# Kernel tuning notes

Measured on AMD Instinct MI355X. Metric: run time of the kernel, lower is better.

## Reference

```python
import jax, jax.numpy as jnp
import numpy as np

N, C, T = 65536, 1000, 2.0

def setup_inputs() -> dict:
    key = jax.random.key(0)
    k1, k2, k3, k4 = jax.random.split(key, 4)
    return {
        "outputs1": jax.random.normal(k1, (N, C), dtype=jnp.float32),
        "outputs2": jax.random.normal(k2, (N, C), dtype=jnp.float32),
        "mimic": jax.random.normal(k3, (N, C), dtype=jnp.float32),
        "targets": jax.random.randint(k4, (N,), 0, C, dtype=jnp.int64),
        "n_test": N,
    }

def _margin(x, targets):
    # top-2 per row; margin = top1 - top2 if target logit equals the max, else 0
    top2, _ = jax.lax.top_k(x, 2)                       # [N, 2]
    tgt_logit = jnp.take_along_axis(x, targets[:, None], axis=1)[:, 0]  # [N]
    return jnp.where(tgt_logit == top2[:, 0], top2[:, 0] - top2[:, 1], 0.0)

def reference(outputs1, outputs2, mimic, targets, n_test):
    d1 = _margin(outputs1, targets)
    d2 = _margin(outputs2, targets)
    m = _margin(mimic, targets)
    preds = jnp.stack([d1, d2, m], axis=1)              # [N, 3]
    out_threshold = jax.nn.softmax(preds / T, axis=1)   # softmax over the 3 margins
    max_preds = jnp.maximum(outputs1.max(), outputs2.max())
    return (max_preds, out_threshold)
```

## Files before the change

kernel.cpp:

```cpp
#include <hip/hip_runtime.h>
#include <math.h>

#define NEG_INF (-__builtin_inff())

__device__ __forceinline__ void top2_update(float v, float& m1, float& m2) {
    float nm1 = fmaxf(m1, v);
    m2 = fmaxf(m2, fminf(m1, v));
    m1 = nm1;
}

__device__ __forceinline__ void upd4(float4 v, float& m1, float& m2) {
    top2_update(v.x, m1, m2); top2_update(v.y, m1, m2);
    top2_update(v.z, m1, m2); top2_update(v.w, m1, m2);
}

__device__ __forceinline__ void top2_merge(float o1, float o2, float& m1, float& m2) {
    float hi = fmaxf(m1, o1);
    float lo = fminf(m1, o1);
    m2 = fmaxf(lo, fmaxf(m2, o2));
    m1 = hi;
}

__device__ __forceinline__ unsigned int enc_float(float f) {
    unsigned int b = __float_as_uint(f);
    return (b & 0x80000000u) ? ~b : (b | 0x80000000u);
}

__global__ __launch_bounds__(256) void margin_softmax_kernel(
    const float* __restrict__ out1,
    const float* __restrict__ out2,
    const float* __restrict__ mim,
    const int*   __restrict__ targets,
    float*       __restrict__ d_out,
    int N)
{
    const int C = 1000;
    const int lane          = threadIdx.x & 63;
    const int wave_in_blk   = threadIdx.x >> 6;
    const int waves_per_blk = blockDim.x >> 6;
    const int gwave  = blockIdx.x * waves_per_blk + wave_in_blk;
    const int nwaves = gridDim.x * waves_per_blk;

    float lane_run = NEG_INF;

    for (int row = gwave; row < N; row += nwaves) {
        const size_t base = (size_t)row * (size_t)C;
        const float4* p1 = (const float4*)(out1 + base);
        const float4* p2 = (const float4*)(out2 + base);
        const float4* p3 = (const float4*)(mim  + base);

        float4 A0 = p1[lane], A1 = p1[lane + 64], A2 = p1[lane + 128];
        float4 B0 = p2[lane], B1 = p2[lane + 64], B2 = p2[lane + 128];
        float4 M0 = p3[lane], M1 = p3[lane + 64], M2 = p3[lane + 128];
        float4 A3 = make_float4(NEG_INF, NEG_INF, NEG_INF, NEG_INF);
        float4 B3 = A3, M3 = A3;
        if (lane < 58) {
            A3 = p1[lane + 192];
            B3 = p2[lane + 192];
            M3 = p3[lane + 192];
        }

        float a1 = NEG_INF, a2 = NEG_INF;
        float b1 = NEG_INF, b2 = NEG_INF;
        float c1 = NEG_INF, c2 = NEG_INF;

        upd4(A0, a1, a2); upd4(A1, a1, a2); upd4(A2, a1, a2); upd4(A3, a1, a2);
        upd4(B0, b1, b2); upd4(B1, b1, b2); upd4(B2, b1, b2); upd4(B3, b1, b2);
        upd4(M0, c1, c2); upd4(M1, c1, c2); upd4(M2, c1, c2); upd4(M3, c1, c2);

        #pragma unroll
        for (int off = 32; off >= 1; off >>= 1) {
            float o1, o2;
            o1 = __shfl_xor(a1, off); o2 = __shfl_xor(a2, off); top2_merge(o1, o2, a1, a2);
            o1 = __shfl_xor(b1, off); o2 = __shfl_xor(b2, off); top2_merge(o1, o2, b1, b2);
            o1 = __shfl_xor(c1, off); o2 = __shfl_xor(c2, off); top2_merge(o1, o2, c1, c2);
        }

        lane_run = fmaxf(lane_run, fmaxf(a1, b1));

        if (lane == 0) {
            int tgt = targets[row];
            float t1 = out1[base + tgt];
            float t2 = out2[base + tgt];
            float t3 = mim [base + tgt];
            float d1 = (t1 == a1) ? (a1 - a2) : 0.0f;
            float d2 = (t2 == b1) ? (b1 - b2) : 0.0f;
            float d3 = (t3 == c1) ? (c1 - c2) : 0.0f;
            float x1 = d1 * 0.5f, x2 = d2 * 0.5f, x3 = d3 * 0.5f;
            float mx = fmaxf(x1, fmaxf(x2, x3));
            float e1 = expf(x1 - mx), e2 = expf(x2 - mx), e3 = expf(x3 - mx);
            float inv = 1.0f / (e1 + e2 + e3);
            float* o = d_out + 1 + (size_t)row * 3;
            o[0] = e1 * inv;
            o[1] = e2 * inv;
            o[2] = e3 * inv;
        }
    }

    #pragma unroll
    for (int off = 32; off >= 1; off >>= 1)
        lane_run = fmaxf(lane_run, __shfl_xor(lane_run, off));

    __shared__ float smax[8];
    if (lane == 0) smax[wave_in_blk] = lane_run;
    __syncthreads();
    if (threadIdx.x == 0) {
        float m = smax[0];
        for (int i = 1; i < waves_per_blk; i++) m = fmaxf(m, smax[i]);
        atomicMax((unsigned int*)d_out, enc_float(m));
    }
}

__global__ void finalize_max_kernel(float* d_out) {
    unsigned int u = ((unsigned int*)d_out)[0];
    unsigned int b = (u & 0x80000000u) ? (u ^ 0x80000000u) : ~u;
    d_out[0] = __uint_as_float(b);
}

extern "C" void kernel_launch(void* const* d_in, const int* in_sizes, int n_in,
                              void* d_out, int out_size, void* d_ws, size_t ws_size,
                              hipStream_t stream) {
    const float* out1    = (const float*)d_in[0];
    const float* out2    = (const float*)d_in[1];
    const float* mim     = (const float*)d_in[2];
    const int*   targets = (const int*)  d_in[3];

    const int N = in_sizes[3];

    (void)hipMemsetAsync(d_out, 0, sizeof(unsigned int), stream);

    margin_softmax_kernel<<<2048, 256, 0, stream>>>(
        out1, out2, mim, targets, (float*)d_out, N);

    finalize_max_kernel<<<1, 1, 0, stream>>>((float*)d_out);
}
```

Measured before the change: 649.3 us.

## Software-pipeline row loads so the next row's data is fetched during current compute

```diff
diff --git a/kernel.cpp b/kernel.cpp
--- a/kernel.cpp
+++ b/kernel.cpp
@@ -14,6 +14,13 @@
     top2_update(v.z, m1, m2); top2_update(v.w, m1, m2);
 }
 
+__device__ __forceinline__ void upd4m(float4 v, bool act, float& m1, float& m2) {
+    top2_update(act ? v.x : NEG_INF, m1, m2);
+    top2_update(act ? v.y : NEG_INF, m1, m2);
+    top2_update(act ? v.z : NEG_INF, m1, m2);
+    top2_update(act ? v.w : NEG_INF, m1, m2);
+}
+
 __device__ __forceinline__ void top2_merge(float o1, float o2, float& m1, float& m2) {
     float hi = fmaxf(m1, o1);
     float lo = fminf(m1, o1);
@@ -24,6 +31,31 @@
 __device__ __forceinline__ unsigned int enc_float(float f) {
     unsigned int b = __float_as_uint(f);
     return (b & 0x80000000u) ? ~b : (b | 0x80000000u);
+}
+
+struct Pending {
+    int    tgt;
+    float4 A0, A1, A2, A3;
+    float4 B0, B1, B2, B3;
+    float4 M0, M1, M2, M3;
+};
+
+__device__ __forceinline__ Pending issue_row(const float* __restrict__ out1,
+                                             const float* __restrict__ out2,
+                                             const float* __restrict__ mim,
+                                             const int*   __restrict__ targets,
+                                             int row, int lane, int tidx)
+{
+    const size_t base = (size_t)row * 1000u;
+    const float4* p1 = (const float4*)(out1 + base);
+    const float4* p2 = (const float4*)(out2 + base);
+    const float4* p3 = (const float4*)(mim  + base);
+    Pending P;
+    P.tgt = targets[row];
+    P.A0 = p1[lane]; P.A1 = p1[lane + 64]; P.A2 = p1[lane + 128]; P.A3 = p1[tidx];
+    P.B0 = p2[lane]; P.B1 = p2[lane + 64]; P.B2 = p2[lane + 128]; P.B3 = p2[tidx];
+    P.M0 = p3[lane]; P.M1 = p3[lane + 64]; P.M2 = p3[lane + 128]; P.M3 = p3[tidx];
+    return P;
 }
 
 __global__ __launch_bounds__(256) void margin_softmax_kernel(
@@ -40,33 +72,33 @@
     const int waves_per_blk = blockDim.x >> 6;
     const int gwave  = blockIdx.x * waves_per_blk + wave_in_blk;
     const int nwaves = gridDim.x * waves_per_blk;
+    const int  tidx = (lane < 58) ? (lane + 192) : lane;
+    const bool tact = (lane < 58);
 
     float lane_run = NEG_INF;
 
-    for (int row = gwave; row < N; row += nwaves) {
+    int row = gwave;
+    Pending cur;
+    if (row < N) cur = issue_row(out1, out2, mim, targets, row, lane, tidx);
+
+    while (row < N) {
         const size_t base = (size_t)row * (size_t)C;
-        const float4* p1 = (const float4*)(out1 + base);
-        const float4* p2 = (const float4*)(out2 + base);
-        const float4* p3 = (const float4*)(mim  + base);
 
-        float4 A0 = p1[lane], A1 = p1[lane + 64], A2 = p1[lane + 128];
-        float4 B0 = p2[lane], B1 = p2[lane + 64], B2 = p2[lane + 128];
-        float4 M0 = p3[lane], M1 = p3[lane + 64], M2 = p3[lane + 128];
-        float4 A3 = make_float4(NEG_INF, NEG_INF, NEG_INF, NEG_INF);
-        float4 B3 = A3, M3 = A3;
-        if (lane < 58) {
-            A3 = p1[lane + 192];
-            B3 = p2[lane + 192];
-            M3 = p3[lane + 192];
-        }
+        const int tgt = cur.tgt;
+        float t1 = out1[base + tgt];
+        float t2 = out2[base + tgt];
+        float t3 = mim [base + tgt];
+
+        const int nrow = row + nwaves;
+        Pending nxt;
+        if (nrow < N) nxt = issue_row(out1, out2, mim, targets, nrow, lane, tidx);
 
         float a1 = NEG_INF, a2 = NEG_INF;
         float b1 = NEG_INF, b2 = NEG_INF;
         float c1 = NEG_INF, c2 = NEG_INF;
-
-        upd4(A0, a1, a2); upd4(A1, a1, a2); upd4(A2, a1, a2); upd4(A3, a1, a2);
-        upd4(B0, b1, b2); upd4(B1, b1, b2); upd4(B2, b1, b2); upd4(B3, b1, b2);
-        upd4(M0, c1, c2); upd4(M1, c1, c2); upd4(M2, c1, c2); upd4(M3, c1, c2);
+        upd4(cur.A0, a1, a2); upd4(cur.A1, a1, a2); upd4(cur.A2, a1, a2); upd4m(cur.A3, tact, a1, a2);
+        upd4(cur.B0, b1, b2); upd4(cur.B1, b1, b2); upd4(cur.B2, b1, b2); upd4m(cur.B3, tact, b1, b2);
+        upd4(cur.M0, c1, c2); upd4(cur.M1, c1, c2); upd4(cur.M2, c1, c2); upd4m(cur.M3, tact, c1, c2);
 
         #pragma unroll
         for (int off = 32; off >= 1; off >>= 1) {
@@ -79,10 +111,6 @@
         lane_run = fmaxf(lane_run, fmaxf(a1, b1));
 
         if (lane == 0) {
-            int tgt = targets[row];
-            float t1 = out1[base + tgt];
-            float t2 = out2[base + tgt];
-            float t3 = mim [base + tgt];
             float d1 = (t1 == a1) ? (a1 - a2) : 0.0f;
             float d2 = (t2 == b1) ? (b1 - b2) : 0.0f;
             float d3 = (t3 == c1) ? (c1 - c2) : 0.0f;
@@ -95,6 +123,9 @@
             o[1] = e2 * inv;
             o[2] = e3 * inv;
         }
+
+        row = nrow;
+        cur = nxt;
     }
 
     #pragma unroll
```

Measured after the change: 650.7 us. About the same (+0.2%).
